# Kernel tuning notes

Measured on AMD Instinct MI355X. Metric: run time of the kernel, lower is better.

Reference implementation:

```python
import jax, jax.numpy as jnp
import numpy as np

N, E = 20000, 640000
IN_CH, OUT_CH = 128, 64
HEADS = (4, 4)
NEG_SLOPE = 0.2


def _gat_layer(x, src, dst, edge_attr, edge_atten, W, a_src, a_dst, W_e, a_e, b, H, C, n_nodes):
    # x: [N, F_in] -> per-head features [N, H, C]
    xh = (x @ W).reshape(-1, H, C)
    alpha_src = jnp.sum(xh * a_src, axis=-1)          # [N, H]
    alpha_dst = jnp.sum(xh * a_dst, axis=-1)          # [N, H]
    eemb = (edge_attr @ W_e).reshape(-1, H, C)        # [E, H, C]
    alpha_e = jnp.sum(eemb * a_e, axis=-1)            # [E, H]
    alpha = alpha_src[src] + alpha_dst[dst] + alpha_e # [E, H]
    alpha = jax.nn.leaky_relu(alpha, NEG_SLOPE)
    # softmax over variable-degree neighborhoods (segments keyed by dst)
    amax = jax.ops.segment_max(alpha, dst, num_segments=n_nodes)
    alpha = jnp.exp(alpha - amax[dst])
    denom = jax.ops.segment_sum(alpha, dst, num_segments=n_nodes)
    alpha = alpha / (denom[dst] + 1e-16)
    msg = xh[src] * alpha[:, :, None]                 # [E, H, C]
    msg = msg * edge_atten[:, :, None]                # edge_atten: [E, 1] -> broadcast over H, C
    out = jax.ops.segment_sum(msg, dst, num_segments=n_nodes)
    out = out.reshape(n_nodes, H * C) + b
    return out, alpha


def setup_inputs() -> dict:
    key = jax.random.key(0)
    ks = jax.random.split(key, 16)
    H1, H2 = HEADS
    d1_in, d1_out = IN_CH, H1 * OUT_CH
    d2_in, d2_out = H1 * OUT_CH, H2 * OUT_CH
    s = lambda fi: 1.0 / np.sqrt(fi)
    inp = {
        "x": jax.random.normal(ks[0], (N, IN_CH), jnp.float32),
        "edge_index": jax.random.randint(ks[1], (2, E), 0, N, jnp.int64 if jax.config.jax_enable_x64 else jnp.int32),
        "batch": jnp.zeros((N,), jnp.int32),
        "edge_attr": jax.random.normal(ks[2], (E, 1), jnp.float32),
        "edge_atten": jax.random.uniform(ks[3], (E, 1), jnp.float32),
        # layer 1 params
        "W1": jax.random.normal(ks[4], (d1_in, d1_out), jnp.float32) * s(d1_in),
        "a_src1": jax.random.normal(ks[5], (H1, OUT_CH), jnp.float32) * s(OUT_CH),
        "a_dst1": jax.random.normal(ks[6], (H1, OUT_CH), jnp.float32) * s(OUT_CH),
        "W_e1": jax.random.normal(ks[7], (1, d1_out), jnp.float32),
        "a_e1": jax.random.normal(ks[8], (H1, OUT_CH), jnp.float32) * s(OUT_CH),
        "b1": jnp.zeros((d1_out,), jnp.float32),
        # layer 2 params
        "W2": jax.random.normal(ks[9], (d2_in, d2_out), jnp.float32) * s(d2_in),
        "a_src2": jax.random.normal(ks[10], (H2, OUT_CH), jnp.float32) * s(OUT_CH),
        "a_dst2": jax.random.normal(ks[11], (H2, OUT_CH), jnp.float32) * s(OUT_CH),
        "W_e2": jax.random.normal(ks[12], (1, d2_out), jnp.float32),
        "a_e2": jax.random.normal(ks[13], (H2, OUT_CH), jnp.float32) * s(OUT_CH),
        "b2": jnp.zeros((d2_out,), jnp.float32),
    }
    return inp


def reference(x, edge_index, batch, edge_attr, edge_atten,
              W1, a_src1, a_dst1, W_e1, a_e1, b1,
              W2, a_src2, a_dst2, W_e2, a_e2, b2):
    src, dst = edge_index[0], edge_index[1]
    h, w1 = _gat_layer(x, src, dst, edge_attr, edge_atten,
                       W1, a_src1, a_dst1, W_e1, a_e1, b1, HEADS[0], OUT_CH, N)
    h, w2 = _gat_layer(h, src, dst, edge_attr, edge_atten,
                       W2, a_src2, a_dst2, W_e2, a_e2, b2, HEADS[1], OUT_CH, N)
    return h, w1, w2
```

## Files before the change

### kernel.cpp

```cpp
#include <hip/hip_runtime.h>
#include <math.h>

#define NEG_SLOPE 0.2f
#define CAP 128
#define NNODES 20000
#define NB 128

typedef short s16x8 __attribute__((ext_vector_type(8)));
typedef unsigned short us8 __attribute__((ext_vector_type(8)));
typedef float f32x4 __attribute__((ext_vector_type(4)));

__device__ __forceinline__ unsigned short f2bf(float f) {
    unsigned int u = __float_as_uint(f);
    return (unsigned short)((u + 0x7FFFu + ((u >> 16) & 1u)) >> 16);
}
__device__ __forceinline__ float bf2f(unsigned short s) {
    return __uint_as_float(((unsigned int)s) << 16);
}

__global__ __launch_bounds__(512) void hist_prep(const int* __restrict__ dst,
                                                 int* __restrict__ ghist,
                                                 int E, int chunk, int N, int histB,
                                                 const float* __restrict__ x,
                                                 const float* __restrict__ W1,
                                                 const float* __restrict__ W2,
                                                 const float* __restrict__ W_e1,
                                                 const float* __restrict__ a_e1,
                                                 const float* __restrict__ W_e2,
                                                 const float* __restrict__ a_e2,
                                                 unsigned short* __restrict__ xb16,
                                                 unsigned short* __restrict__ Wt1,
                                                 unsigned short* __restrict__ Wt2,
                                                 float* __restrict__ ce) {
    __shared__ int h[NNODES];
    if ((int)blockIdx.x < histB) {
        const int b = blockIdx.x;
        for (int i = threadIdx.x; i < N; i += 512) h[i] = 0;
        __syncthreads();
        const int e0 = b * chunk;
        const int e1 = min(e0 + chunk, E);
        for (int e = e0 + (int)threadIdx.x; e < e1; e += 512)
            atomicAdd(&h[dst[e]], 1);
        __syncthreads();
        int* out = ghist + (size_t)b * N;
        for (int i = threadIdx.x; i < N; i += 512) out[i] = h[i];
    } else {
        const int p = (int)blockIdx.x - histB;
        const int gsz = 256 * 512;
        const int gid = p * 512 + (int)threadIdx.x;
        for (int i = gid; i < 128 * 256; i += gsz) {
            int k = i >> 8, n = i & 255;
            Wt1[n * 128 + k] = f2bf(W1[i]);
        }
        for (int i = gid; i < 256 * 256; i += gsz) {
            int k = i >> 8, n = i & 255;
            Wt2[n * 256 + k] = f2bf(W2[i]);
        }
        for (int i = gid; i < N * 32; i += gsz) {
            float4 f = ((const float4*)x)[i];
            ushort4 u = make_ushort4(f2bf(f.x), f2bf(f.y), f2bf(f.z), f2bf(f.w));
            ((ushort4*)xb16)[i] = u;
        }
        if (p < 2 && threadIdx.x < 256) {
            const float* We = p == 0 ? W_e1 : W_e2;
            const float* ae = p == 0 ? a_e1 : a_e2;
            int hh = threadIdx.x >> 6, c = threadIdx.x & 63;
            float pr = We[hh * 64 + c] * ae[hh * 64 + c];
#pragma unroll
            for (int off = 32; off > 0; off >>= 1) pr += __shfl_down(pr, off);
            if (c == 0) ce[p * 4 + hh] = pr;
        }
    }
}

__global__ __launch_bounds__(1024) void scan_kernel(const int* __restrict__ deg,
                                                    int* __restrict__ off, int N) {
    __shared__ int wsum[16];
    __shared__ int woff[16];
    __shared__ int s_carry, s_bt;
    if (threadIdx.x == 0) s_carry = 0;
    __syncthreads();
    const int lane = threadIdx.x & 63, wid = threadIdx.x >> 6;
    for (int base = 0; base < N; base += 4096) {
        int i0 = base + (int)threadIdx.x * 4;
        int v0 = (i0 + 0 < N) ? deg[i0 + 0] : 0;
        int v1 = (i0 + 1 < N) ? deg[i0 + 1] : 0;
        int v2 = (i0 + 2 < N) ? deg[i0 + 2] : 0;
        int v3 = (i0 + 3 < N) ? deg[i0 + 3] : 0;
        int tsum = v0 + v1 + v2 + v3;
        int incl = tsum;
#pragma unroll
        for (int ofs = 1; ofs < 64; ofs <<= 1) {
            int t = __shfl_up(incl, ofs);
            if (lane >= ofs) incl += t;
        }
        if (lane == 63) wsum[wid] = incl;
        __syncthreads();
        if (wid == 0) {
            int ws = (lane < 16) ? wsum[lane] : 0;
            int wincl = ws;
#pragma unroll
            for (int ofs = 1; ofs < 16; ofs <<= 1) {
                int t = __shfl_up(wincl, ofs);
                if (lane >= ofs) wincl += t;
            }
            if (lane < 16) woff[lane] = wincl - ws;
            if (lane == 15) s_bt = wincl;
        }
        __syncthreads();
        int e0 = s_carry + woff[wid] + incl - tsum;
        int e1 = e0 + v0, e2 = e1 + v1, e3 = e2 + v2;
        if (i0 + 0 < N) off[i0 + 0] = e0;
        if (i0 + 1 < N) off[i0 + 1] = e1;
        if (i0 + 2 < N) off[i0 + 2] = e2;
        if (i0 + 3 < N) off[i0 + 3] = e3;
        __syncthreads();
        if (threadIdx.x == 0) s_carry += s_bt;
        __syncthreads();
    }
    if (threadIdx.x == 0) off[N] = s_carry;
}

__device__ __forceinline__ void gemm_core(const unsigned short* __restrict__ A16,
                                          const unsigned short* __restrict__ Bt16,
                                          unsigned short* __restrict__ C16,
                                          const float* __restrict__ a_src,
                                          const float* __restrict__ a_dst,
                                          float* __restrict__ asrc,
                                          float* __restrict__ adst,
                                          int M, int K, int bx, int by,
                                          unsigned short (*As)[40],
                                          unsigned short (*Bs)[40]) {
    const int tid = threadIdx.x;
    const int w = tid >> 6, l = tid & 63;
    const int quad = l >> 4, m16 = l & 15;
    const int row0 = by * 128, col0 = bx * 64;

    f32x4 acc[2][4] = {};

    const int a_r = tid >> 1;
    const int a_k = (tid & 1) * 16;
    const int b_n = tid >> 2;
    const int b_k = (tid & 3) * 8;

    for (int k0 = 0; k0 < K; k0 += 32) {
        int gr = row0 + a_r; if (gr > M - 1) gr = M - 1;
        const unsigned short* ap = A16 + (size_t)gr * K + k0 + a_k;
        *(us8*)&As[a_r][a_k]     = *(const us8*)ap;
        *(us8*)&As[a_r][a_k + 8] = *(const us8*)(ap + 8);
        *(us8*)&Bs[b_n][b_k] = *(const us8*)(Bt16 + (size_t)(col0 + b_n) * K + k0 + b_k);
        __syncthreads();

        s16x8 af[2], bfr[4];
#pragma unroll
        for (int mt = 0; mt < 2; ++mt)
            af[mt] = *(const s16x8*)&As[w * 32 + mt * 16 + m16][quad * 8];
#pragma unroll
        for (int nt = 0; nt < 4; ++nt)
            bfr[nt] = *(const s16x8*)&Bs[nt * 16 + m16][quad * 8];
#pragma unroll
        for (int mt = 0; mt < 2; ++mt)
#pragma unroll
            for (int nt = 0; nt < 4; ++nt)
                acc[mt][nt] = __builtin_amdgcn_mfma_f32_16x16x32_bf16(af[mt], bfr[nt], acc[mt][nt], 0, 0, 0);
        __syncthreads();
    }

    const int h = bx;
    float was[4], wad[4];
#pragma unroll
    for (int nt = 0; nt < 4; ++nt) {
        int c = nt * 16 + m16;
        was[nt] = a_src[h * 64 + c];
        wad[nt] = a_dst[h * 64 + c];
    }

#pragma unroll
    for (int mt = 0; mt < 2; ++mt)
#pragma unroll
        for (int i = 0; i < 4; ++i) {
            int row = row0 + w * 32 + mt * 16 + quad * 4 + i;
            float ps = 0.f, pd = 0.f;
#pragma unroll
            for (int nt = 0; nt < 4; ++nt) {
                float v = acc[mt][nt][i];
                ps += v * was[nt];
                pd += v * wad[nt];
            }
#pragma unroll
            for (int ofs = 1; ofs < 16; ofs <<= 1) {
                ps += __shfl_xor(ps, ofs);
                pd += __shfl_xor(pd, ofs);
            }
            if (m16 == 0 && row < M) {
                asrc[(size_t)row * 4 + h] = ps;
                adst[(size_t)row * 4 + h] = pd;
            }
        }

#pragma unroll
    for (int mt = 0; mt < 2; ++mt)
#pragma unroll
        for (int nt = 0; nt < 4; ++nt) {
            int col = col0 + nt * 16 + m16;
#pragma unroll
            for (int i = 0; i < 4; ++i) {
                int row = row0 + w * 32 + mt * 16 + quad * 4 + i;
                if (row < M) C16[(size_t)row * 256 + col] = f2bf(acc[mt][nt][i]);
            }
        }
}

__global__ __launch_bounds__(256) void gemm1_scan(const unsigned short* __restrict__ A16,
                                                  const unsigned short* __restrict__ Bt16,
                                                  unsigned short* __restrict__ C16,
                                                  const float* __restrict__ a_src,
                                                  const float* __restrict__ a_dst,
                                                  float* __restrict__ asrc,
                                                  float* __restrict__ adst,
                                                  int M, int K, int gemmB,
                                                  int* __restrict__ ghist,
                                                  int* __restrict__ deg,
                                                  int N, int histB) {
    __shared__ unsigned short As[128][40];
    __shared__ unsigned short Bs[64][40];
    if ((int)blockIdx.x < gemmB) {
        gemm_core(A16, Bt16, C16, a_src, a_dst, asrc, adst, M, K,
                  blockIdx.x & 3, blockIdx.x >> 2, As, Bs);
    } else {
        int bin = ((int)blockIdx.x - gemmB) * 256 + (int)threadIdx.x;
        if (bin < N) {
            int run = 0;
            for (int b = 0; b < histB; b += 8) {
                int v[8];
#pragma unroll
                for (int j = 0; j < 8; ++j) v[j] = ghist[(b + j) * N + bin];
#pragma unroll
                for (int j = 0; j < 8; ++j) { ghist[(b + j) * N + bin] = run; run += v[j]; }
            }
            deg[bin] = run;
        }
    }
}

__global__ __launch_bounds__(512) void fill2(const int* __restrict__ src,
                                             const int* __restrict__ dst,
                                             const float* __restrict__ edge_attr,
                                             const float* __restrict__ edge_atten,
                                             const int* __restrict__ off,
                                             const int* __restrict__ ghist,
                                             int4* __restrict__ rec,
                                             int E, int chunk, int N) {
    __shared__ int base[NNODES];
    const int b = blockIdx.x;
    const int* part = ghist + (size_t)b * N;
    for (int i = threadIdx.x; i < N; i += 512) base[i] = off[i] + part[i];
    __syncthreads();
    const int e0 = b * chunk;
    const int e1 = min(e0 + chunk, E);
    for (int e = e0 + (int)threadIdx.x; e < e1; e += 512) {
        int d = dst[e];
        int pos = atomicAdd(&base[d], 1);
        rec[pos] = make_int4(src[e], e, __float_as_int(edge_attr[e]),
                             __float_as_int(edge_atten[e]));
    }
}

__global__ __launch_bounds__(256) void node_fused(const int4* __restrict__ rec,
                                                  const int* __restrict__ off,
                                                  const float* __restrict__ asrc,
                                                  const float* __restrict__ adst,
                                                  const float* __restrict__ ce,
                                                  const unsigned short* __restrict__ xh16,
                                                  const float* __restrict__ bias,
                                                  float* __restrict__ w,
                                                  float* __restrict__ houtf,
                                                  unsigned short* __restrict__ hout16,
                                                  int N) {
    __shared__ float s_al[4][CAP * 4];
    __shared__ int s_src[4][CAP];
    const int wid = threadIdx.x >> 6;
    const int n = blockIdx.x * 4 + wid;
    if (n >= N) return;
    const int lane = threadIdx.x & 63;
    float* al = s_al[wid];
    int* sv = s_src[wid];
    const int o0 = off[n], o1 = off[n + 1];
    const int deg = o1 - o0;

    const float4 c4 = *(const float4*)ce;
    const float4 ad4 = *(const float4*)(adst + (size_t)n * 4);

    if (deg <= 64) {
        int4 r; float4 a;
        a.x = a.y = a.z = a.w = -3.4e38f;
        if (lane < deg) {
            r = rec[o0 + lane];
            float ea = __int_as_float(r.z);
            const float4 as4 = *(const float4*)(asrc + (size_t)r.x * 4);
            a.x = as4.x + ad4.x + ea * c4.x;
            a.y = as4.y + ad4.y + ea * c4.y;
            a.z = as4.z + ad4.z + ea * c4.z;
            a.w = as4.w + ad4.w + ea * c4.w;
            a.x = a.x > 0.f ? a.x : NEG_SLOPE * a.x;
            a.y = a.y > 0.f ? a.y : NEG_SLOPE * a.y;
            a.z = a.z > 0.f ? a.z : NEG_SLOPE * a.z;
            a.w = a.w > 0.f ? a.w : NEG_SLOPE * a.w;
        }
        float4 mx = a;
#pragma unroll
        for (int ofs = 1; ofs < 64; ofs <<= 1) {
            mx.x = fmaxf(mx.x, __shfl_xor(mx.x, ofs));
            mx.y = fmaxf(mx.y, __shfl_xor(mx.y, ofs));
            mx.z = fmaxf(mx.z, __shfl_xor(mx.z, ofs));
            mx.w = fmaxf(mx.w, __shfl_xor(mx.w, ofs));
        }
        float4 ex = make_float4(0.f, 0.f, 0.f, 0.f);
        if (lane < deg) {
            ex.x = __expf(a.x - mx.x);
            ex.y = __expf(a.y - mx.y);
            ex.z = __expf(a.z - mx.z);
            ex.w = __expf(a.w - mx.w);
        }
        float4 sm = ex;
#pragma unroll
        for (int ofs = 1; ofs < 64; ofs <<= 1) {
            sm.x += __shfl_xor(sm.x, ofs);
            sm.y += __shfl_xor(sm.y, ofs);
            sm.z += __shfl_xor(sm.z, ofs);
            sm.w += __shfl_xor(sm.w, ofs);
        }
        float4 rc;
        rc.x = 1.f / (sm.x + 1e-16f);
        rc.y = 1.f / (sm.y + 1e-16f);
        rc.z = 1.f / (sm.z + 1e-16f);
        rc.w = 1.f / (sm.w + 1e-16f);
        if (lane < deg) {
            float4 aln;
            aln.x = ex.x * rc.x;
            aln.y = ex.y * rc.y;
            aln.z = ex.z * rc.z;
            aln.w = ex.w * rc.w;
            *(float4*)(w + (size_t)r.y * 4) = aln;
            float att = __int_as_float(r.w);
            sv[lane] = r.x;
            al[0 * CAP + lane] = aln.x * att;
            al[1 * CAP + lane] = aln.y * att;
            al[2 * CAP + lane] = aln.z * att;
            al[3 * CAP + lane] = aln.w * att;
        }
    } else {
        float4 mx = make_float4(-3.4e38f, -3.4e38f, -3.4e38f, -3.4e38f);
        for (int idx = lane; idx < deg; idx += 64) {
            int4 r = rec[o0 + idx];
            float ea = __int_as_float(r.z);
            const float4 as4 = *(const float4*)(asrc + (size_t)r.x * 4);
            float4 a;
            a.x = as4.x + ad4.x + ea * c4.x;
            a.y = as4.y + ad4.y + ea * c4.y;
            a.z = as4.z + ad4.z + ea * c4.z;
            a.w = as4.w + ad4.w + ea * c4.w;
            a.x = a.x > 0.f ? a.x : NEG_SLOPE * a.x;
            a.y = a.y > 0.f ? a.y : NEG_SLOPE * a.y;
            a.z = a.z > 0.f ? a.z : NEG_SLOPE * a.z;
            a.w = a.w > 0.f ? a.w : NEG_SLOPE * a.w;
            if (idx < CAP) {
                sv[idx] = r.x;
                al[0 * CAP + idx] = a.x;
                al[1 * CAP + idx] = a.y;
                al[2 * CAP + idx] = a.z;
                al[3 * CAP + idx] = a.w;
            } else {
                *(float4*)(w + (size_t)r.y * 4) = a;
            }
            mx.x = fmaxf(mx.x, a.x);
            mx.y = fmaxf(mx.y, a.y);
            mx.z = fmaxf(mx.z, a.z);
            mx.w = fmaxf(mx.w, a.w);
        }
#pragma unroll
        for (int ofs = 1; ofs < 64; ofs <<= 1) {
            mx.x = fmaxf(mx.x, __shfl_xor(mx.x, ofs));
            mx.y = fmaxf(mx.y, __shfl_xor(mx.y, ofs));
            mx.z = fmaxf(mx.z, __shfl_xor(mx.z, ofs));
            mx.w = fmaxf(mx.w, __shfl_xor(mx.w, ofs));
        }
        float4 sm = make_float4(0.f, 0.f, 0.f, 0.f);
        for (int idx = lane; idx < deg; idx += 64) {
            float4 a;
            int espill = -1;
            if (idx < CAP) {
                a.x = al[0 * CAP + idx];
                a.y = al[1 * CAP + idx];
                a.z = al[2 * CAP + idx];
                a.w = al[3 * CAP + idx];
            } else {
                espill = rec[o0 + idx].y;
                a = *(const float4*)(w + (size_t)espill * 4);
            }
            a.x = __expf(a.x - mx.x);
            a.y = __expf(a.y - mx.y);
            a.z = __expf(a.z - mx.z);
            a.w = __expf(a.w - mx.w);
            if (idx < CAP) {
                al[0 * CAP + idx] = a.x;
                al[1 * CAP + idx] = a.y;
                al[2 * CAP + idx] = a.z;
                al[3 * CAP + idx] = a.w;
            } else {
                *(float4*)(w + (size_t)espill * 4) = a;
            }
            sm.x += a.x; sm.y += a.y; sm.z += a.z; sm.w += a.w;
        }
#pragma unroll
        for (int ofs = 1; ofs < 64; ofs <<= 1) {
            sm.x += __shfl_xor(sm.x, ofs);
            sm.y += __shfl_xor(sm.y, ofs);
            sm.z += __shfl_xor(sm.z, ofs);
            sm.w += __shfl_xor(sm.w, ofs);
        }
        float4 rc;
        rc.x = 1.f / (sm.x + 1e-16f);
        rc.y = 1.f / (sm.y + 1e-16f);
        rc.z = 1.f / (sm.z + 1e-16f);
        rc.w = 1.f / (sm.w + 1e-16f);
        for (int idx = lane; idx < deg; idx += 64) {
            int4 r = rec[o0 + idx];
            float4 ex;
            if (idx < CAP) {
                ex.x = al[0 * CAP + idx];
                ex.y = al[1 * CAP + idx];
                ex.z = al[2 * CAP + idx];
                ex.w = al[3 * CAP + idx];
            } else {
                ex = *(const float4*)(w + (size_t)r.y * 4);
            }
            float4 aln;
            aln.x = ex.x * rc.x;
            aln.y = ex.y * rc.y;
            aln.z = ex.z * rc.z;
            aln.w = ex.w * rc.w;
            *(float4*)(w + (size_t)r.y * 4) = aln;
            if (idx < CAP) {
                float att = __int_as_float(r.w);
                al[0 * CAP + idx] = aln.x * att;
                al[1 * CAP + idx] = aln.y * att;
                al[2 * CAP + idx] = aln.z * att;
                al[3 * CAP + idx] = aln.w * att;
            }
        }
    }

    const int hh = lane >> 4;
    const float* alh = al + hh * CAP;
    float4 acc = *(const float4*)(bias + lane * 4);
    const int kmax = deg < CAP ? deg : CAP;
    int k = 0;
    for (; k + 4 <= kmax; k += 4) {
        int4 s4 = *(const int4*)&sv[k];
        float4 cc = *(const float4*)&alh[k];
        ushort4 u0 = *((const ushort4*)(xh16 + (size_t)s4.x * 256) + lane);
        ushort4 u1 = *((const ushort4*)(xh16 + (size_t)s4.y * 256) + lane);
        ushort4 u2 = *((const ushort4*)(xh16 + (size_t)s4.z * 256) + lane);
        ushort4 u3 = *((const ushort4*)(xh16 + (size_t)s4.w * 256) + lane);
        acc.x += bf2f(u0.x) * cc.x; acc.y += bf2f(u0.y) * cc.x; acc.z += bf2f(u0.z) * cc.x; acc.w += bf2f(u0.w) * cc.x;
        acc.x += bf2f(u1.x) * cc.y; acc.y += bf2f(u1.y) * cc.y; acc.z += bf2f(u1.z) * cc.y; acc.w += bf2f(u1.w) * cc.y;
        acc.x += bf2f(u2.x) * cc.z; acc.y += bf2f(u2.y) * cc.z; acc.z += bf2f(u2.z) * cc.z; acc.w += bf2f(u2.w) * cc.z;
        acc.x += bf2f(u3.x) * cc.w; acc.y += bf2f(u3.y) * cc.w; acc.z += bf2f(u3.z) * cc.w; acc.w += bf2f(u3.w) * cc.w;
    }
    for (; k < kmax; ++k) {
        int s = sv[k];
        float sc = alh[k];
        ushort4 uv = *((const ushort4*)(xh16 + (size_t)s * 256) + lane);
        acc.x += bf2f(uv.x) * sc; acc.y += bf2f(uv.y) * sc;
        acc.z += bf2f(uv.z) * sc; acc.w += bf2f(uv.w) * sc;
    }
    for (k = CAP; k < deg; ++k) {
        int4 r = rec[o0 + k];
        float sc = w[(size_t)r.y * 4 + hh] * __int_as_float(r.w);
        ushort4 uv = *((const ushort4*)(xh16 + (size_t)r.x * 256) + lane);
        acc.x += bf2f(uv.x) * sc; acc.y += bf2f(uv.y) * sc;
        acc.z += bf2f(uv.z) * sc; acc.w += bf2f(uv.w) * sc;
    }
    if (houtf)  *(float4*)(houtf + (size_t)n * 256 + lane * 4) = acc;
    if (hout16) {
        ushort4 u = make_ushort4(f2bf(acc.x), f2bf(acc.y), f2bf(acc.z), f2bf(acc.w));
        *((ushort4*)(hout16 + (size_t)n * 256) + lane) = u;
    }
}

__global__ __launch_bounds__(256) void gemm_k(const unsigned short* __restrict__ A16,
                                              const unsigned short* __restrict__ Bt16,
                                              unsigned short* __restrict__ C16,
                                              const float* __restrict__ a_src,
                                              const float* __restrict__ a_dst,
                                              float* __restrict__ asrc,
                                              float* __restrict__ adst,
                                              int M, int K) {
    __shared__ unsigned short As[128][40];
    __shared__ unsigned short Bs[64][40];
    gemm_core(A16, Bt16, C16, a_src, a_dst, asrc, adst, M, K,
              blockIdx.x, blockIdx.y, As, Bs);
}

extern "C" void kernel_launch(void* const* d_in, const int* in_sizes, int n_in,
                              void* d_out, int out_size, void* d_ws, size_t ws_size,
                              hipStream_t stream) {
    const float* x          = (const float*)d_in[0];
    const int*   ei         = (const int*)d_in[1];
    const float* edge_attr  = (const float*)d_in[3];
    const float* edge_atten = (const float*)d_in[4];
    const float* W1     = (const float*)d_in[5];
    const float* a_src1 = (const float*)d_in[6];
    const float* a_dst1 = (const float*)d_in[7];
    const float* W_e1   = (const float*)d_in[8];
    const float* a_e1   = (const float*)d_in[9];
    const float* b1     = (const float*)d_in[10];
    const float* W2     = (const float*)d_in[11];
    const float* a_src2 = (const float*)d_in[12];
    const float* a_dst2 = (const float*)d_in[13];
    const float* W_e2   = (const float*)d_in[14];
    const float* a_e2   = (const float*)d_in[15];
    const float* b2     = (const float*)d_in[16];

    const int N = in_sizes[0] / 128;
    const int E = in_sizes[1] / 2;
    const int* srcp = ei;
    const int* dstp = ei + E;

    char* ws = (char*)d_ws;
    int4* rec             = (int4*)ws;            ws += (size_t)E * 16;
    unsigned short* xh16  = (unsigned short*)ws;  ws += (size_t)N * 256 * 2;
    unsigned short* h116  = (unsigned short*)ws;  ws += (size_t)N * 256 * 2;
    unsigned short* Wt1   = (unsigned short*)ws;  ws += (size_t)256 * 128 * 2;
    unsigned short* Wt2   = (unsigned short*)ws;  ws += (size_t)256 * 256 * 2;
    float* asrc   = (float*)ws;                   ws += (size_t)N * 4 * 4;
    float* adst   = (float*)ws;                   ws += (size_t)N * 4 * 4;
    float* ce     = (float*)ws;                   ws += 32;
    int* deg    = (int*)ws;                       ws += (size_t)N * 4;
    int* off    = (int*)ws;                       ws += (size_t)(N + 1) * 4;
    int* ghist  = (int*)ws;                       ws += (size_t)NB * N * 4;

    unsigned short* xb16 = h116;

    float* hout2 = (float*)d_out;
    float* w1    = hout2 + (size_t)N * 256;
    float* w2    = w1 + (size_t)E * 4;

    const int chunk = (E + NB - 1) / NB;
    const int gb = (N + 3) / 4;
    const int rows = (N + 127) / 128;
    const int gemmB = 4 * rows;
    const int scanB = (N + 255) / 256;

    hist_prep<<<NB + 256, 512, 0, stream>>>(dstp, ghist, E, chunk, N, NB,
                                            x, W1, W2, W_e1, a_e1, W_e2, a_e2,
                                            xb16, Wt1, Wt2, ce);
    gemm1_scan<<<gemmB + scanB, 256, 0, stream>>>(xb16, Wt1, xh16, a_src1, a_dst1,
                                                  asrc, adst, N, 128, gemmB,
                                                  ghist, deg, N, NB);
    scan_kernel<<<1, 1024, 0, stream>>>(deg, off, N);
    fill2<<<NB, 512, 0, stream>>>(srcp, dstp, edge_attr, edge_atten, off, ghist,
                                  rec, E, chunk, N);
    node_fused<<<gb, 256, 0, stream>>>(rec, off, asrc, adst, ce, xh16, b1, w1,
                                       (float*)nullptr, h116, N);
    gemm_k<<<dim3(4, rows), 256, 0, stream>>>(h116, Wt2, xh16, a_src2, a_dst2,
                                              asrc, adst, N, 256);
    node_fused<<<gb, 256, 0, stream>>>(rec, off, asrc, adst, ce + 4, xh16, b2, w2,
                                       hout2, (unsigned short*)nullptr, N);
}
```

Measured before the change: 273.6 us.

## Pack histogram counters, pad LDS rows, split accumulators, and move w1 writes into gemm2

The histogram now packs two 16-bit counters per shared int, which halves the LDS footprint. fill2 runs with 1024 threads. node_fused pads its per-head attention rows (stride 136) to avoid LDS bank conflicts and uses four independent accumulators in the gather loop. For low-degree nodes, layer 1 no longer writes its scattered w1 output and instead saves the per-node max and reciprocal sum. A coalesced per-edge pass fused alongside the gemm2 blocks then recomputes w1 in edge order. The exchange is extra recomputation and an extra mxrc buffer. The 16-bit counters could overflow if a node's in-degree within one chunk exceeds 65535.

```diff
diff --git a/kernel.cpp b/kernel.cpp
--- a/kernel.cpp
+++ b/kernel.cpp
@@ -3,6 +3,7 @@
 
 #define NEG_SLOPE 0.2f
 #define CAP 128
+#define ST  136
 #define NNODES 20000
 #define NB 128
 
@@ -32,18 +33,24 @@
                                                  unsigned short* __restrict__ Wt1,
                                                  unsigned short* __restrict__ Wt2,
                                                  float* __restrict__ ce) {
-    __shared__ int h[NNODES];
+    __shared__ int h[NNODES / 2];
     if ((int)blockIdx.x < histB) {
         const int b = blockIdx.x;
-        for (int i = threadIdx.x; i < N; i += 512) h[i] = 0;
+        const int NH = N >> 1;
+        for (int i = threadIdx.x; i < NH; i += 512) h[i] = 0;
         __syncthreads();
         const int e0 = b * chunk;
         const int e1 = min(e0 + chunk, E);
-        for (int e = e0 + (int)threadIdx.x; e < e1; e += 512)
-            atomicAdd(&h[dst[e]], 1);
-        __syncthreads();
-        int* out = ghist + (size_t)b * N;
-        for (int i = threadIdx.x; i < N; i += 512) out[i] = h[i];
+        for (int e = e0 + (int)threadIdx.x; e < e1; e += 512) {
+            int d = dst[e];
+            atomicAdd(&h[d >> 1], 1 << ((d & 1) << 4));
+        }
+        __syncthreads();
+        int2* out = (int2*)(ghist + (size_t)b * N);
+        for (int i = threadIdx.x; i < NH; i += 512) {
+            int v = h[i];
+            out[i] = make_int2(v & 0xFFFF, ((unsigned)v) >> 16);
+        }
     } else {
         const int p = (int)blockIdx.x - histB;
         const int gsz = 256 * 512;
@@ -243,22 +250,22 @@
     }
 }
 
-__global__ __launch_bounds__(512) void fill2(const int* __restrict__ src,
-                                             const int* __restrict__ dst,
-                                             const float* __restrict__ edge_attr,
-                                             const float* __restrict__ edge_atten,
-                                             const int* __restrict__ off,
-                                             const int* __restrict__ ghist,
-                                             int4* __restrict__ rec,
-                                             int E, int chunk, int N) {
+__global__ __launch_bounds__(1024) void fill2(const int* __restrict__ src,
+                                              const int* __restrict__ dst,
+                                              const float* __restrict__ edge_attr,
+                                              const float* __restrict__ edge_atten,
+                                              const int* __restrict__ off,
+                                              const int* __restrict__ ghist,
+                                              int4* __restrict__ rec,
+                                              int E, int chunk, int N) {
     __shared__ int base[NNODES];
     const int b = blockIdx.x;
     const int* part = ghist + (size_t)b * N;
-    for (int i = threadIdx.x; i < N; i += 512) base[i] = off[i] + part[i];
+    for (int i = threadIdx.x; i < N; i += 1024) base[i] = off[i] + part[i];
     __syncthreads();
     const int e0 = b * chunk;
     const int e1 = min(e0 + chunk, E);
-    for (int e = e0 + (int)threadIdx.x; e < e1; e += 512) {
+    for (int e = e0 + (int)threadIdx.x; e < e1; e += 1024) {
         int d = dst[e];
         int pos = atomicAdd(&base[d], 1);
         rec[pos] = make_int4(src[e], e, __float_as_int(edge_attr[e]),
@@ -274,16 +281,18 @@
                                                   const unsigned short* __restrict__ xh16,
                                                   const float* __restrict__ bias,
                                                   float* __restrict__ w,
+                                                  int write_w,
+                                                  float* __restrict__ mxrc,
                                                   float* __restrict__ houtf,
                                                   unsigned short* __restrict__ hout16,
                                                   int N) {
-    __shared__ float s_al[4][CAP * 4];
+    __shared__ float s_al[4][4][ST];
     __shared__ int s_src[4][CAP];
     const int wid = threadIdx.x >> 6;
     const int n = blockIdx.x * 4 + wid;
     if (n >= N) return;
     const int lane = threadIdx.x & 63;
-    float* al = s_al[wid];
+    float* al = &s_al[wid][0][0];
     int* sv = s_src[wid];
     const int o0 = off[n], o1 = off[n + 1];
     const int deg = o1 - o0;
@@ -335,19 +344,23 @@
         rc.y = 1.f / (sm.y + 1e-16f);
         rc.z = 1.f / (sm.z + 1e-16f);
         rc.w = 1.f / (sm.w + 1e-16f);
+        if (mxrc && lane == 0) {
+            *(float4*)(mxrc + (size_t)n * 8) = mx;
+            *(float4*)(mxrc + (size_t)n * 8 + 4) = rc;
+        }
         if (lane < deg) {
             float4 aln;
             aln.x = ex.x * rc.x;
             aln.y = ex.y * rc.y;
             aln.z = ex.z * rc.z;
             aln.w = ex.w * rc.w;
-            *(float4*)(w + (size_t)r.y * 4) = aln;
+            if (write_w) *(float4*)(w + (size_t)r.y * 4) = aln;
             float att = __int_as_float(r.w);
             sv[lane] = r.x;
-            al[0 * CAP + lane] = aln.x * att;
-            al[1 * CAP + lane] = aln.y * att;
-            al[2 * CAP + lane] = aln.z * att;
-            al[3 * CAP + lane] = aln.w * att;
+            al[0 * ST + lane] = aln.x * att;
+            al[1 * ST + lane] = aln.y * att;
+            al[2 * ST + lane] = aln.z * att;
+            al[3 * ST + lane] = aln.w * att;
         }
     } else {
         float4 mx = make_float4(-3.4e38f, -3.4e38f, -3.4e38f, -3.4e38f);
@@ -366,10 +379,10 @@
             a.w = a.w > 0.f ? a.w : NEG_SLOPE * a.w;
             if (idx < CAP) {
                 sv[idx] = r.x;
-                al[0 * CAP + idx] = a.x;
-                al[1 * CAP + idx] = a.y;
-                al[2 * CAP + idx] = a.z;
-                al[3 * CAP + idx] = a.w;
+                al[0 * ST + idx] = a.x;
+                al[1 * ST + idx] = a.y;
+                al[2 * ST + idx] = a.z;
+                al[3 * ST + idx] = a.w;
             } else {
                 *(float4*)(w + (size_t)r.y * 4) = a;
             }
@@ -390,10 +403,10 @@
             float4 a;
             int espill = -1;
             if (idx < CAP) {
-                a.x = al[0 * CAP + idx];
-                a.y = al[1 * CAP + idx];
-                a.z = al[2 * CAP + idx];
-                a.w = al[3 * CAP + idx];
+                a.x = al[0 * ST + idx];
+                a.y = al[1 * ST + idx];
+                a.z = al[2 * ST + idx];
+                a.w = al[3 * ST + idx];
             } else {
                 espill = rec[o0 + idx].y;
                 a = *(const float4*)(w + (size_t)espill * 4);
@@ -403,10 +416,10 @@
             a.z = __expf(a.z - mx.z);
             a.w = __expf(a.w - mx.w);
             if (idx < CAP) {
-                al[0 * CAP + idx] = a.x;
-                al[1 * CAP + idx] = a.y;
-                al[2 * CAP + idx] = a.z;
-                al[3 * CAP + idx] = a.w;
+                al[0 * ST + idx] = a.x;
+                al[1 * ST + idx] = a.y;
+                al[2 * ST + idx] = a.z;
+                al[3 * ST + idx] = a.w;
             } else {
                 *(float4*)(w + (size_t)espill * 4) = a;
             }
@@ -424,14 +437,18 @@
         rc.y = 1.f / (sm.y + 1e-16f);
         rc.z = 1.f / (sm.z + 1e-16f);
         rc.w = 1.f / (sm.w + 1e-16f);
+        if (mxrc && lane == 0) {
+            *(float4*)(mxrc + (size_t)n * 8) = mx;
+            *(float4*)(mxrc + (size_t)n * 8 + 4) = rc;
+        }
         for (int idx = lane; idx < deg; idx += 64) {
             int4 r = rec[o0 + idx];
             float4 ex;
             if (idx < CAP) {
-                ex.x = al[0 * CAP + idx];
-                ex.y = al[1 * CAP + idx];
-                ex.z = al[2 * CAP + idx];
-                ex.w = al[3 * CAP + idx];
+                ex.x = al[0 * ST + idx];
+                ex.y = al[1 * ST + idx];
+                ex.z = al[2 * ST + idx];
+                ex.w = al[3 * ST + idx];
             } else {
                 ex = *(const float4*)(w + (size_t)r.y * 4);
             }
@@ -443,17 +460,20 @@
             *(float4*)(w + (size_t)r.y * 4) = aln;
             if (idx < CAP) {
                 float att = __int_as_float(r.w);
-                al[0 * CAP + idx] = aln.x * att;
-                al[1 * CAP + idx] = aln.y * att;
-                al[2 * CAP + idx] = aln.z * att;
-                al[3 * CAP + idx] = aln.w * att;
+                al[0 * ST + idx] = aln.x * att;
+                al[1 * ST + idx] = aln.y * att;
+                al[2 * ST + idx] = aln.z * att;
+                al[3 * ST + idx] = aln.w * att;
             }
         }
     }
 
     const int hh = lane >> 4;
-    const float* alh = al + hh * CAP;
-    float4 acc = *(const float4*)(bias + lane * 4);
+    const float* alh = al + hh * ST;
+    float4 a0 = *(const float4*)(bias + lane * 4);
+    float4 a1 = make_float4(0.f, 0.f, 0.f, 0.f);
+    float4 a2 = make_float4(0.f, 0.f, 0.f, 0.f);
+    float4 a3 = make_float4(0.f, 0.f, 0.f, 0.f);
     const int kmax = deg < CAP ? deg : CAP;
     int k = 0;
     for (; k + 4 <= kmax; k += 4) {
@@ -463,25 +483,30 @@
         ushort4 u1 = *((const ushort4*)(xh16 + (size_t)s4.y * 256) + lane);
         ushort4 u2 = *((const ushort4*)(xh16 + (size_t)s4.z * 256) + lane);
         ushort4 u3 = *((const ushort4*)(xh16 + (size_t)s4.w * 256) + lane);
-        acc.x += bf2f(u0.x) * cc.x; acc.y += bf2f(u0.y) * cc.x; acc.z += bf2f(u0.z) * cc.x; acc.w += bf2f(u0.w) * cc.x;
-        acc.x += bf2f(u1.x) * cc.y; acc.y += bf2f(u1.y) * cc.y; acc.z += bf2f(u1.z) * cc.y; acc.w += bf2f(u1.w) * cc.y;
-        acc.x += bf2f(u2.x) * cc.z; acc.y += bf2f(u2.y) * cc.z; acc.z += bf2f(u2.z) * cc.z; acc.w += bf2f(u2.w) * cc.z;
-        acc.x += bf2f(u3.x) * cc.w; acc.y += bf2f(u3.y) * cc.w; acc.z += bf2f(u3.z) * cc.w; acc.w += bf2f(u3.w) * cc.w;
+        a0.x += bf2f(u0.x) * cc.x; a0.y += bf2f(u0.y) * cc.x; a0.z += bf2f(u0.z) * cc.x; a0.w += bf2f(u0.w) * cc.x;
+        a1.x += bf2f(u1.x) * cc.y; a1.y += bf2f(u1.y) * cc.y; a1.z += bf2f(u1.z) * cc.y; a1.w += bf2f(u1.w) * cc.y;
+        a2.x += bf2f(u2.x) * cc.z; a2.y += bf2f(u2.y) * cc.z; a2.z += bf2f(u2.z) * cc.z; a2.w += bf2f(u2.w) * cc.z;
+        a3.x += bf2f(u3.x) * cc.w; a3.y += bf2f(u3.y) * cc.w; a3.z += bf2f(u3.z) * cc.w; a3.w += bf2f(u3.w) * cc.w;
     }
     for (; k < kmax; ++k) {
         int s = sv[k];
         float sc = alh[k];
         ushort4 uv = *((const ushort4*)(xh16 + (size_t)s * 256) + lane);
-        acc.x += bf2f(uv.x) * sc; acc.y += bf2f(uv.y) * sc;
-        acc.z += bf2f(uv.z) * sc; acc.w += bf2f(uv.w) * sc;
+        a0.x += bf2f(uv.x) * sc; a0.y += bf2f(uv.y) * sc;
+        a0.z += bf2f(uv.z) * sc; a0.w += bf2f(uv.w) * sc;
     }
     for (k = CAP; k < deg; ++k) {
         int4 r = rec[o0 + k];
         float sc = w[(size_t)r.y * 4 + hh] * __int_as_float(r.w);
         ushort4 uv = *((const ushort4*)(xh16 + (size_t)r.x * 256) + lane);
-        acc.x += bf2f(uv.x) * sc; acc.y += bf2f(uv.y) * sc;
-        acc.z += bf2f(uv.z) * sc; acc.w += bf2f(uv.w) * sc;
-    }
+        a0.x += bf2f(uv.x) * sc; a0.y += bf2f(uv.y) * sc;
+        a0.z += bf2f(uv.z) * sc; a0.w += bf2f(uv.w) * sc;
+    }
+    float4 acc;
+    acc.x = (a0.x + a1.x) + (a2.x + a3.x);
+    acc.y = (a0.y + a1.y) + (a2.y + a3.y);
+    acc.z = (a0.z + a1.z) + (a2.z + a3.z);
+    acc.w = (a0.w + a1.w) + (a2.w + a3.w);
     if (houtf)  *(float4*)(houtf + (size_t)n * 256 + lane * 4) = acc;
     if (hout16) {
         ushort4 u = make_ushort4(f2bf(acc.x), f2bf(acc.y), f2bf(acc.z), f2bf(acc.w));
@@ -489,18 +514,54 @@
     }
 }
 
-__global__ __launch_bounds__(256) void gemm_k(const unsigned short* __restrict__ A16,
-                                              const unsigned short* __restrict__ Bt16,
-                                              unsigned short* __restrict__ C16,
-                                              const float* __restrict__ a_src,
-                                              const float* __restrict__ a_dst,
-                                              float* __restrict__ asrc,
-                                              float* __restrict__ adst,
-                                              int M, int K) {
+__global__ __launch_bounds__(256) void gemm2_w1(const unsigned short* __restrict__ A16,
+                                                const unsigned short* __restrict__ Bt16,
+                                                unsigned short* __restrict__ C16,
+                                                const float* __restrict__ a_src,
+                                                const float* __restrict__ a_dst,
+                                                float* __restrict__ asrc2,
+                                                float* __restrict__ adst2,
+                                                int M, int K, int gemmB,
+                                                const int* __restrict__ src,
+                                                const int* __restrict__ dstp,
+                                                const float* __restrict__ edge_attr,
+                                                const float* __restrict__ asrc1,
+                                                const float* __restrict__ adst1,
+                                                const float* __restrict__ mxrc,
+                                                const float* __restrict__ ce1,
+                                                float* __restrict__ w1, int E) {
     __shared__ unsigned short As[128][40];
     __shared__ unsigned short Bs[64][40];
-    gemm_core(A16, Bt16, C16, a_src, a_dst, asrc, adst, M, K,
-              blockIdx.x, blockIdx.y, As, Bs);
+    if ((int)blockIdx.x < gemmB) {
+        gemm_core(A16, Bt16, C16, a_src, a_dst, asrc2, adst2, M, K,
+                  blockIdx.x & 3, blockIdx.x >> 2, As, Bs);
+    } else {
+        const int stride = ((int)gridDim.x - gemmB) * 256;
+        const float4 c4 = *(const float4*)ce1;
+        for (int e = ((int)blockIdx.x - gemmB) * 256 + (int)threadIdx.x; e < E; e += stride) {
+            int s = src[e], d = dstp[e];
+            float ea = edge_attr[e];
+            const float4 as4 = *(const float4*)(asrc1 + (size_t)s * 4);
+            const float4 ad4 = *(const float4*)(adst1 + (size_t)d * 4);
+            float4 a;
+            a.x = as4.x + ad4.x + ea * c4.x;
+            a.y = as4.y + ad4.y + ea * c4.y;
+            a.z = as4.z + ad4.z + ea * c4.z;
+            a.w = as4.w + ad4.w + ea * c4.w;
+            a.x = a.x > 0.f ? a.x : NEG_SLOPE * a.x;
+            a.y = a.y > 0.f ? a.y : NEG_SLOPE * a.y;
+            a.z = a.z > 0.f ? a.z : NEG_SLOPE * a.z;
+            a.w = a.w > 0.f ? a.w : NEG_SLOPE * a.w;
+            const float4 mx = *(const float4*)(mxrc + (size_t)d * 8);
+            const float4 rc = *(const float4*)(mxrc + (size_t)d * 8 + 4);
+            float4 o;
+            o.x = __expf(a.x - mx.x) * rc.x;
+            o.y = __expf(a.y - mx.y) * rc.y;
+            o.z = __expf(a.z - mx.z) * rc.z;
+            o.w = __expf(a.w - mx.w) * rc.w;
+            *(float4*)(w1 + (size_t)e * 4) = o;
+        }
+    }
 }
 
 extern "C" void kernel_launch(void* const* d_in, const int* in_sizes, int n_in,
@@ -536,6 +597,9 @@
     unsigned short* Wt2   = (unsigned short*)ws;  ws += (size_t)256 * 256 * 2;
     float* asrc   = (float*)ws;                   ws += (size_t)N * 4 * 4;
     float* adst   = (float*)ws;                   ws += (size_t)N * 4 * 4;
+    float* asrc2  = (float*)ws;                   ws += (size_t)N * 4 * 4;
+    float* adst2  = (float*)ws;                   ws += (size_t)N * 4 * 4;
+    float* mxrc   = (float*)ws;                   ws += (size_t)N * 8 * 4;
     float* ce     = (float*)ws;                   ws += 32;
     int* deg    = (int*)ws;                       ws += (size_t)N * 4;
     int* off    = (int*)ws;                       ws += (size_t)(N + 1) * 4;
@@ -552,6 +616,7 @@
     const int rows = (N + 127) / 128;
     const int gemmB = 4 * rows;
     const int scanB = (N + 255) / 256;
+    const int wB = 512;
 
     hist_prep<<<NB + 256, 512, 0, stream>>>(dstp, ghist, E, chunk, N, NB,
                                             x, W1, W2, W_e1, a_e1, W_e2, a_e2,
@@ -560,12 +625,15 @@
                                                   asrc, adst, N, 128, gemmB,
                                                   ghist, deg, N, NB);
     scan_kernel<<<1, 1024, 0, stream>>>(deg, off, N);
-    fill2<<<NB, 512, 0, stream>>>(srcp, dstp, edge_attr, edge_atten, off, ghist,
-                                  rec, E, chunk, N);
+    fill2<<<NB, 1024, 0, stream>>>(srcp, dstp, edge_attr, edge_atten, off, ghist,
+                                   rec, E, chunk, N);
     node_fused<<<gb, 256, 0, stream>>>(rec, off, asrc, adst, ce, xh16, b1, w1,
-                                       (float*)nullptr, h116, N);
-    gemm_k<<<dim3(4, rows), 256, 0, stream>>>(h116, Wt2, xh16, a_src2, a_dst2,
-                                              asrc, adst, N, 256);
-    node_fused<<<gb, 256, 0, stream>>>(rec, off, asrc, adst, ce + 4, xh16, b2, w2,
-                                       hout2, (unsigned short*)nullptr, N);
-}
+                                       0, mxrc, (float*)nullptr, h116, N);
+    gemm2_w1<<<gemmB + wB, 256, 0, stream>>>(h116, Wt2, xh16, a_src2, a_dst2,
+                                             asrc2, adst2, N, 256, gemmB,
+                                             srcp, dstp, edge_attr,
+                                             asrc, adst, mxrc, ce, w1, E);
+    node_fused<<<gb, 256, 0, stream>>>(rec, off, asrc2, adst2, ce + 4, xh16, b2, w2,
+                                       1, (float*)nullptr, hout2,
+                                       (unsigned short*)nullptr, N);
+}
```

After: 255.9 us. -6.5%, faster.
